# Kernel optimization log

Measured on AMD Instinct MI355X. Metric: run time of the kernel, lower is better.

## Reference

```python
import jax, jax.numpy as jnp
import numpy as np

B, R, H, W = 8, 128, 4096, 4096

def setup_inputs() -> dict:
    key = jax.random.key(0)
    k1, k2, k3, k4 = jax.random.split(key, 4)
    N = jax.random.normal(k1, (B, 1, R, W), dtype=jnp.float32)
    Ak_L = jax.random.normal(k2, (B, 1, H, W), dtype=jnp.float32)
    alpha = jax.random.uniform(k3, (B,), dtype=jnp.float32)
    gamma = jax.random.uniform(k4, (B,), dtype=jnp.float32)
    return {"N": N, "Ak_L": Ak_L, "alpha": alpha, "gamma": gamma}

def reference(N, Ak_L, alpha, gamma):
    # N: [B,1,r,W], Ak_L: [B,1,H,W], alpha/gamma: [B]
    b = N.shape[0]
    r = N.shape[2]
    a = alpha.reshape(b, 1, 1, 1)
    g = gamma.reshape(b, 1, 1, 1)
    I = jnp.eye(r, dtype=N.dtype)  # broadcast over [B,1,r,r]
    # C = alpha*I + 2*gamma * N @ N^T  -> [B,1,r,r]
    C = a * I + 2.0 * g * jnp.einsum('bcrw,bcsw->bcrs', N, N)
    Cinv = jnp.linalg.pinv(C)  # batched pinv over [B,1]
    # X = (Ak_L @ N^T) @ pinv(C) -> [B,1,H,r]
    AN = jnp.einsum('bchw,bcrw->bchr', Ak_L, N)
    X = jnp.einsum('bchr,bcrs->bchs', AN, Cinv)
    return 2.0 * g * X
```

## Files before the change

### kernel.cpp

```cpp
#include <hip/hip_runtime.h>


typedef __attribute__((ext_vector_type(8))) short bf16x8;
typedef __attribute__((ext_vector_type(4))) float f32x4;
typedef __attribute__((ext_vector_type(4))) unsigned int u32x4;

#define MFMA16(a, b, c) __builtin_amdgcn_mfma_f32_16x16x32_bf16((a), (b), (c), 0, 0, 0)
#define NSPLIT 8

__device__ __forceinline__ unsigned short f2bf(float f) {
  union { float f; unsigned u; } v; v.f = f;
  unsigned u = v.u;
  return (unsigned short)((u + 0x7FFFu + ((u >> 16) & 1u)) >> 16);
}
__device__ __forceinline__ unsigned pack2(float x, float y) {
  return (unsigned)f2bf(x) | ((unsigned)f2bf(y) << 16);
}

__global__ __launch_bounds__(256) void k_castT(const float* __restrict__ N,
                                               unsigned short* __restrict__ NT) {
  __attribute__((aligned(16))) __shared__ float tile[128 * 68];
  int wc = blockIdx.x, b = blockIdx.y;
  const float* Nb = N + (size_t)b * 524288 + wc * 64;
  int t = threadIdx.x;
  int row = t >> 1, half = t & 1;
  const float* src = Nb + (size_t)row * 4096 + half * 32;
  float* dst = tile + row * 68 + half * 32;
#pragma unroll
  for (int j = 0; j < 8; j++) *(f32x4*)(dst + j * 4) = *(const f32x4*)(src + j * 4);
  __syncthreads();
  int ow = t >> 2, q = t & 3;
  unsigned short* out = NT + (size_t)b * 524288 + (size_t)(wc * 64 + ow) * 128 + q * 32;
#pragma unroll
  for (int c = 0; c < 4; c++) {
    u32x4 p;
#pragma unroll
    for (int k = 0; k < 4; k++) {
      float f0 = tile[(q * 32 + c * 8 + k * 2) * 68 + ow];
      float f1 = tile[(q * 32 + c * 8 + k * 2 + 1) * 68 + ow];
      p[k] = pack2(f0, f1);
    }
    *(u32x4*)(out + c * 8) = p;
  }
}

__global__ __launch_bounds__(256) void k_gram(const float* __restrict__ N,
                                              float* __restrict__ Gpart) {
  __attribute__((aligned(16))) __shared__ unsigned short lds[128 * 72];
  int ks = blockIdx.x, b = blockIdx.y;
  const float* Nb = N + (size_t)b * 524288 + ks * 512;
  int t = threadIdx.x;
  int wave = t >> 6, lane = t & 63, quad = lane >> 4, l16 = lane & 15;
  f32x4 acc[2][8];
#pragma unroll
  for (int i = 0; i < 2; i++)
#pragma unroll
    for (int j = 0; j < 8; j++) acc[i][j] = (f32x4){0.f, 0.f, 0.f, 0.f};
  int srow = t >> 1, shalf = t & 1;
  const float* srcb = Nb + (size_t)srow * 4096 + shalf * 32;
  unsigned short* dptr = lds + srow * 72 + shalf * 32;
  for (int it = 0; it < 8; ++it) {
    u32x4 pk0, pk1;
    {
      f32x4 v0 = *(const f32x4*)(srcb + it * 64 + 0);
      f32x4 v1 = *(const f32x4*)(srcb + it * 64 + 4);
      f32x4 v2 = *(const f32x4*)(srcb + it * 64 + 8);
      f32x4 v3 = *(const f32x4*)(srcb + it * 64 + 12);
      pk0[0] = pack2(v0[0], v0[1]); pk0[1] = pack2(v0[2], v0[3]);
      pk0[2] = pack2(v1[0], v1[1]); pk0[3] = pack2(v1[2], v1[3]);
      pk1[0] = pack2(v2[0], v2[1]); pk1[1] = pack2(v2[2], v2[3]);
      pk1[2] = pack2(v3[0], v3[1]); pk1[3] = pack2(v3[2], v3[3]);
    }
    u32x4 pk2, pk3;
    {
      f32x4 v0 = *(const f32x4*)(srcb + it * 64 + 16);
      f32x4 v1 = *(const f32x4*)(srcb + it * 64 + 20);
      f32x4 v2 = *(const f32x4*)(srcb + it * 64 + 24);
      f32x4 v3 = *(const f32x4*)(srcb + it * 64 + 28);
      pk2[0] = pack2(v0[0], v0[1]); pk2[1] = pack2(v0[2], v0[3]);
      pk2[2] = pack2(v1[0], v1[1]); pk2[3] = pack2(v1[2], v1[3]);
      pk3[0] = pack2(v2[0], v2[1]); pk3[1] = pack2(v2[2], v2[3]);
      pk3[2] = pack2(v3[0], v3[1]); pk3[3] = pack2(v3[2], v3[3]);
    }
    __syncthreads();
    *(u32x4*)(dptr + 0) = pk0;
    *(u32x4*)(dptr + 8) = pk1;
    *(u32x4*)(dptr + 16) = pk2;
    *(u32x4*)(dptr + 24) = pk3;
    __syncthreads();
    bf16x8 af[2][2], bfv[8][2];
#pragma unroll
    for (int mt = 0; mt < 2; mt++)
#pragma unroll
      for (int kk = 0; kk < 2; kk++)
        af[mt][kk] = *(const bf16x8*)(lds + (wave * 32 + mt * 16 + l16) * 72 + (kk * 4 + quad) * 8);
#pragma unroll
    for (int nt = 0; nt < 8; nt++)
#pragma unroll
      for (int kk = 0; kk < 2; kk++)
        bfv[nt][kk] = *(const bf16x8*)(lds + (nt * 16 + l16) * 72 + (kk * 4 + quad) * 8);
#pragma unroll
    for (int mt = 0; mt < 2; mt++)
#pragma unroll
      for (int nt = 0; nt < 8; nt++)
#pragma unroll
        for (int kk = 0; kk < 2; kk++)
          acc[mt][nt] = MFMA16(af[mt][kk], bfv[nt][kk], acc[mt][nt]);
  }
  float* Gp = Gpart + ((size_t)(b * NSPLIT + ks) << 14);
#pragma unroll
  for (int mt = 0; mt < 2; mt++)
#pragma unroll
    for (int nt = 0; nt < 8; nt++)
#pragma unroll
      for (int rg = 0; rg < 4; rg++) {
        int row = wave * 32 + mt * 16 + quad * 4 + rg;
        int col = nt * 16 + l16;
        Gp[row * 128 + col] = acc[mt][nt][rg];
      }
}

__global__ __launch_bounds__(1024) void k_inv(const float* __restrict__ Gpart,
                                              const float* __restrict__ alpha,
                                              const float* __restrict__ gamma,
                                              float* __restrict__ Cinv) {
  __attribute__((aligned(16))) __shared__ float Cs[16384];
  __attribute__((aligned(16))) __shared__ float mcol[2][128];
  __attribute__((aligned(16))) __shared__ float pivrow[2][128];
  int b = blockIdx.x;
  int t = threadIdx.x;
  const float* Gp = Gpart + ((size_t)b * NSPLIT << 14);
#pragma unroll
  for (int c = 0; c < 4; c++) {
    int off = c * 4096 + t * 4;
    f32x4 s = (f32x4){0.f, 0.f, 0.f, 0.f};
#pragma unroll
    for (int ks = 0; ks < NSPLIT; ks++) s += *(const f32x4*)(Gp + ks * 16384 + off);
    *(f32x4*)(Cs + off) = s;
  }
  __syncthreads();
  int cg = t & 31, rb = t >> 5;
  float al = alpha[b], ga2 = 2.f * gamma[b];
  float a[4][4];
#pragma unroll
  for (int i = 0; i < 4; i++) {
    int r = rb * 4 + i;
    f32x4 v = *(const f32x4*)(Cs + r * 128 + cg * 4);
#pragma unroll
    for (int j = 0; j < 4; j++) {
      int c = cg * 4 + j;
      a[i][j] = ga2 * v[j] + ((r == c) ? al : 0.f);
    }
  }
  for (int p = 0; p < 128; ++p) {
    int pb = p & 1;
    int cgp = p >> 2, jp = p & 3;
    int rbp = p >> 2, ip = p & 3;
    if (cg == cgp) {
      f32x4 mv;
#pragma unroll
      for (int i = 0; i < 4; i++)
        mv[i] = (jp & 2) ? ((jp & 1) ? a[i][3] : a[i][2]) : ((jp & 1) ? a[i][1] : a[i][0]);
      *(f32x4*)&mcol[pb][rb * 4] = mv;
    }
    if (rb == rbp) {
      f32x4 pv;
#pragma unroll
      for (int j = 0; j < 4; j++)
        pv[j] = (ip & 2) ? ((ip & 1) ? a[3][j] : a[2][j]) : ((ip & 1) ? a[1][j] : a[0][j]);
      *(f32x4*)&pivrow[pb][cg * 4] = pv;
    }
    __syncthreads();
    float invd = 1.0f / mcol[pb][p];
    f32x4 mc = *(const f32x4*)&mcol[pb][rb * 4];
    f32x4 pr = *(const f32x4*)&pivrow[pb][cg * 4];
#pragma unroll
    for (int i = 0; i < 4; i++) {
      int r = rb * 4 + i;
      float mi = mc[i] * invd;
#pragma unroll
      for (int j = 0; j < 4; j++) {
        int c = cg * 4 + j;
        float v = a[i][j] - mi * pr[j];
        if (c == p) v = -mi;
        if (r == p) v = pr[j] * invd;
        if (r == p && c == p) v = invd;
        a[i][j] = v;
      }
    }
  }
  float* dst = Cinv + ((size_t)b << 14);
#pragma unroll
  for (int i = 0; i < 4; i++) {
    int r = rb * 4 + i;
    *(f32x4*)(dst + r * 128 + cg * 4) = (f32x4){a[i][0], a[i][1], a[i][2], a[i][3]};
  }
}

__global__ __launch_bounds__(256) void k_mt(const float* __restrict__ Cinv,
                                            const unsigned short* __restrict__ NT,
                                            const float* __restrict__ gamma,
                                            unsigned short* __restrict__ Mt) {
  __attribute__((aligned(16))) __shared__ unsigned short la[128 * 72];
  __attribute__((aligned(16))) __shared__ unsigned short lb[128 * 72];
  int wc = blockIdx.x, b = blockIdx.y;
  int w0 = wc * 128;
  float ga2 = 2.f * gamma[b];
  const float* Cb = Cinv + ((size_t)b << 14);
  const unsigned short* NTb = NT + (size_t)b * 524288;
  int t = threadIdx.x, wave = t >> 6, lane = t & 63, quad = lane >> 4, l16 = lane & 15;
  f32x4 acc[2][8];
#pragma unroll
  for (int i = 0; i < 2; i++)
#pragma unroll
    for (int j = 0; j < 8; j++) acc[i][j] = (f32x4){0.f, 0.f, 0.f, 0.f};
  int row = t >> 1, half = t & 1;
  const float* asrc = Cb + (size_t)row * 128 + half * 32;
  const unsigned short* bsrc = NTb + (size_t)(w0 + row) * 128 + half * 32;
  unsigned short* adst = la + row * 72 + half * 32;
  unsigned short* bdst = lb + row * 72 + half * 32;
  for (int it = 0; it < 2; ++it) {
    int k0 = it * 64;
    u32x4 pa0, pa1;
    {
      f32x4 v0 = *(const f32x4*)(asrc + k0 + 0);
      f32x4 v1 = *(const f32x4*)(asrc + k0 + 4);
      f32x4 v2 = *(const f32x4*)(asrc + k0 + 8);
      f32x4 v3 = *(const f32x4*)(asrc + k0 + 12);
      pa0[0] = pack2(ga2 * v0[0], ga2 * v0[1]); pa0[1] = pack2(ga2 * v0[2], ga2 * v0[3]);
      pa0[2] = pack2(ga2 * v1[0], ga2 * v1[1]); pa0[3] = pack2(ga2 * v1[2], ga2 * v1[3]);
      pa1[0] = pack2(ga2 * v2[0], ga2 * v2[1]); pa1[1] = pack2(ga2 * v2[2], ga2 * v2[3]);
      pa1[2] = pack2(ga2 * v3[0], ga2 * v3[1]); pa1[3] = pack2(ga2 * v3[2], ga2 * v3[3]);
    }
    u32x4 pa2, pa3;
    {
      f32x4 v0 = *(const f32x4*)(asrc + k0 + 16);
      f32x4 v1 = *(const f32x4*)(asrc + k0 + 20);
      f32x4 v2 = *(const f32x4*)(asrc + k0 + 24);
      f32x4 v3 = *(const f32x4*)(asrc + k0 + 28);
      pa2[0] = pack2(ga2 * v0[0], ga2 * v0[1]); pa2[1] = pack2(ga2 * v0[2], ga2 * v0[3]);
      pa2[2] = pack2(ga2 * v1[0], ga2 * v1[1]); pa2[3] = pack2(ga2 * v1[2], ga2 * v1[3]);
      pa3[0] = pack2(ga2 * v2[0], ga2 * v2[1]); pa3[1] = pack2(ga2 * v2[2], ga2 * v2[3]);
      pa3[2] = pack2(ga2 * v3[0], ga2 * v3[1]); pa3[3] = pack2(ga2 * v3[2], ga2 * v3[3]);
    }
    u32x4 bv0 = *(const u32x4*)(bsrc + k0 + 0);
    u32x4 bv1 = *(const u32x4*)(bsrc + k0 + 8);
    u32x4 bv2 = *(const u32x4*)(bsrc + k0 + 16);
    u32x4 bv3 = *(const u32x4*)(bsrc + k0 + 24);
    __syncthreads();
    *(u32x4*)(adst + 0) = pa0;  *(u32x4*)(adst + 8) = pa1;
    *(u32x4*)(adst + 16) = pa2; *(u32x4*)(adst + 24) = pa3;
    *(u32x4*)(bdst + 0) = bv0;  *(u32x4*)(bdst + 8) = bv1;
    *(u32x4*)(bdst + 16) = bv2; *(u32x4*)(bdst + 24) = bv3;
    __syncthreads();
    bf16x8 af[2][2], bfv[8][2];
#pragma unroll
    for (int mt = 0; mt < 2; mt++)
#pragma unroll
      for (int kk = 0; kk < 2; kk++)
        af[mt][kk] = *(const bf16x8*)(la + (wave * 32 + mt * 16 + l16) * 72 + (kk * 4 + quad) * 8);
#pragma unroll
    for (int nt = 0; nt < 8; nt++)
#pragma unroll
      for (int kk = 0; kk < 2; kk++)
        bfv[nt][kk] = *(const bf16x8*)(lb + (nt * 16 + l16) * 72 + (kk * 4 + quad) * 8);
#pragma unroll
    for (int mt = 0; mt < 2; mt++)
#pragma unroll
      for (int nt = 0; nt < 8; nt++)
#pragma unroll
        for (int kk = 0; kk < 2; kk++)
          acc[mt][nt] = MFMA16(af[mt][kk], bfv[nt][kk], acc[mt][nt]);
    __syncthreads();
  }
  unsigned short* Mb = Mt + (size_t)b * 524288;
#pragma unroll
  for (int mt = 0; mt < 2; mt++)
#pragma unroll
    for (int nt = 0; nt < 8; nt++)
#pragma unroll
      for (int rg = 0; rg < 4; rg++) {
        int r = wave * 32 + mt * 16 + quad * 4 + rg;
        int w = w0 + nt * 16 + l16;
        Mb[(size_t)r * 4096 + w] = f2bf(acc[mt][nt][rg]);
      }
}

__device__ __forceinline__ void gemm_step(
    f32x4& A0, f32x4& A1, f32x4& A2, f32x4& A3,
    u32x4& B0, u32x4& B1, u32x4& B2, u32x4& B3,
    unsigned short* adst, unsigned short* bdst,
    const unsigned short* lap, const unsigned short* lbp,
    const float* asrc, const unsigned short* bsrc,
    int next_k0, int do_pf, int wm, int wr, int quad, int l16,
    f32x4 (&acc)[2][4]) {
  u32x4 pa0, pa1;
  pa0[0] = pack2(A0[0], A0[1]); pa0[1] = pack2(A0[2], A0[3]);
  pa0[2] = pack2(A1[0], A1[1]); pa0[3] = pack2(A1[2], A1[3]);
  pa1[0] = pack2(A2[0], A2[1]); pa1[1] = pack2(A2[2], A2[3]);
  pa1[2] = pack2(A3[0], A3[1]); pa1[3] = pack2(A3[2], A3[3]);
  *(u32x4*)(adst + 0) = pa0;
  *(u32x4*)(adst + 8) = pa1;
  *(u32x4*)(bdst + 0) = B0;
  *(u32x4*)(bdst + 8) = B1;
  *(u32x4*)(bdst + 16) = B2;
  *(u32x4*)(bdst + 24) = B3;
  asm volatile("s_waitcnt lgkmcnt(0)" ::: "memory");
  __builtin_amdgcn_s_barrier();
  __builtin_amdgcn_sched_barrier(0);
  if (do_pf) {
    A0 = *(const f32x4*)(asrc + next_k0 + 0);
    A1 = *(const f32x4*)(asrc + next_k0 + 4);
    A2 = *(const f32x4*)(asrc + next_k0 + 8);
    A3 = *(const f32x4*)(asrc + next_k0 + 12);
    B0 = *(const u32x4*)(bsrc + next_k0 + 0);
    B1 = *(const u32x4*)(bsrc + next_k0 + 8);
    B2 = *(const u32x4*)(bsrc + next_k0 + 16);
    B3 = *(const u32x4*)(bsrc + next_k0 + 24);
  }
  bf16x8 af[2][2], bfv[4][2];
#pragma unroll
  for (int mt = 0; mt < 2; mt++)
#pragma unroll
    for (int kk = 0; kk < 2; kk++)
      af[mt][kk] = *(const bf16x8*)(lap + (wm * 32 + mt * 16 + l16) * 72 + (kk * 4 + quad) * 8);
#pragma unroll
  for (int rt = 0; rt < 4; rt++)
#pragma unroll
    for (int kk = 0; kk < 2; kk++)
      bfv[rt][kk] = *(const bf16x8*)(lbp + (wr * 64 + rt * 16 + l16) * 72 + (kk * 4 + quad) * 8);
#pragma unroll
  for (int mt = 0; mt < 2; mt++)
#pragma unroll
    for (int rt = 0; rt < 4; rt++)
#pragma unroll
      for (int kk = 0; kk < 2; kk++)
        acc[mt][rt] = MFMA16(af[mt][kk], bfv[rt][kk], acc[mt][rt]);
}

__global__ __launch_bounds__(256) void k_gemm(const float* __restrict__ A,
                                              const unsigned short* __restrict__ Mt,
                                              float* __restrict__ out) {
  __attribute__((aligned(16))) __shared__ unsigned short la[2][64 * 72];
  __attribute__((aligned(16))) __shared__ unsigned short lb[2][128 * 72];
  int blk = blockIdx.x;
  int b = blk & 7, mtile = blk >> 3;
  const float* Ab = A + (size_t)b * 16777216 + (size_t)mtile * 64 * 4096;
  const unsigned short* Mb = Mt + (size_t)b * 524288;
  int t = threadIdx.x, wave = t >> 6, lane = t & 63, quad = lane >> 4, l16 = lane & 15;
  int wm = wave >> 1, wr = wave & 1;
  f32x4 acc[2][4];
#pragma unroll
  for (int i = 0; i < 2; i++)
#pragma unroll
    for (int j = 0; j < 4; j++) acc[i][j] = (f32x4){0.f, 0.f, 0.f, 0.f};
  int arow = t >> 2, aq = t & 3;
  int brow = t >> 1, bhalf = t & 1;
  const float* asrc = Ab + (size_t)arow * 4096 + aq * 16;
  const unsigned short* bsrc = Mb + (size_t)brow * 4096 + bhalf * 32;
  unsigned short* adst0 = &la[0][arow * 72 + aq * 16];
  unsigned short* adst1 = &la[1][arow * 72 + aq * 16];
  unsigned short* bdst0 = &lb[0][brow * 72 + bhalf * 32];
  unsigned short* bdst1 = &lb[1][brow * 72 + bhalf * 32];
  f32x4 xa0 = *(const f32x4*)(asrc + 0);
  f32x4 xa1 = *(const f32x4*)(asrc + 4);
  f32x4 xa2 = *(const f32x4*)(asrc + 8);
  f32x4 xa3 = *(const f32x4*)(asrc + 12);
  u32x4 xb0 = *(const u32x4*)(bsrc + 0);
  u32x4 xb1 = *(const u32x4*)(bsrc + 8);
  u32x4 xb2 = *(const u32x4*)(bsrc + 16);
  u32x4 xb3 = *(const u32x4*)(bsrc + 24);
  f32x4 ya0 = *(const f32x4*)(asrc + 64);
  f32x4 ya1 = *(const f32x4*)(asrc + 68);
  f32x4 ya2 = *(const f32x4*)(asrc + 72);
  f32x4 ya3 = *(const f32x4*)(asrc + 76);
  u32x4 yb0 = *(const u32x4*)(bsrc + 64);
  u32x4 yb1 = *(const u32x4*)(bsrc + 72);
  u32x4 yb2 = *(const u32x4*)(bsrc + 80);
  u32x4 yb3 = *(const u32x4*)(bsrc + 88);
  for (int itp = 0; itp < 32; ++itp) {
    int pf = (itp < 31);
    gemm_step(xa0, xa1, xa2, xa3, xb0, xb1, xb2, xb3,
              adst0, bdst0, &la[0][0], &lb[0][0], asrc, bsrc,
              (2 * itp + 2) * 64, pf, wm, wr, quad, l16, acc);
    gemm_step(ya0, ya1, ya2, ya3, yb0, yb1, yb2, yb3,
              adst1, bdst1, &la[1][0], &lb[1][0], asrc, bsrc,
              (2 * itp + 3) * 64, pf, wm, wr, quad, l16, acc);
  }
  float* ob = out + (size_t)b * 524288 + (size_t)mtile * 64 * 128;
#pragma unroll
  for (int mt = 0; mt < 2; mt++)
#pragma unroll
    for (int rt = 0; rt < 4; rt++)
#pragma unroll
      for (int rg = 0; rg < 4; rg++) {
        int h = wm * 32 + mt * 16 + quad * 4 + rg;
        int r = wr * 64 + rt * 16 + l16;
        ob[h * 128 + r] = acc[mt][rt][rg];
      }
}

extern "C" void kernel_launch(void* const* d_in, const int* in_sizes, int n_in,
                              void* d_out, int out_size, void* d_ws, size_t ws_size,
                              hipStream_t stream) {
  const float* N = (const float*)d_in[0];
  const float* Ak = (const float*)d_in[1];
  const float* alpha = (const float*)d_in[2];
  const float* gamma = (const float*)d_in[3];
  float* out = (float*)d_out;
  char* ws = (char*)d_ws;
  unsigned short* NT = (unsigned short*)(ws);
  float* Gpart = (float*)(ws + 8388608);
  float* Cinv = (float*)(ws + 12582912);
  unsigned short* Mt = (unsigned short*)(ws + 13107200);

  k_castT<<<dim3(64, 8), 256, 0, stream>>>(N, NT);
  k_gram<<<dim3(NSPLIT, 8), 256, 0, stream>>>(N, Gpart);
  k_inv<<<dim3(8), 1024, 0, stream>>>(Gpart, alpha, gamma, Cinv);
  k_mt<<<dim3(32, 8), 256, 0, stream>>>(Cinv, NT, gamma, Mt);
  k_gemm<<<dim3(512), 256, 0, stream>>>(Ak, Mt, out);
}
```

Measured before the change: 854.5 us.

## Reassociate to (A·Nᵀ)·C⁻¹ and run inversion concurrently with the big GEMM

The pipeline changes from computing M = γ·C⁻¹·N first and then A·Mᵀ to computing AN = A·Nᵀ directly and multiplying by C⁻¹ in a small final kernel. This lets the 128×128 Gauss-Jordan inversion run in 8 extra blocks of the same launch as the large GEMM, so the serial inversion overlaps the GEMM instead of blocking it. The bf16 cast of N is fused into the Gram kernel, which removes the transpose kernel. The big GEMM now uses a PAD of 68, prefetches B one step ahead and A two steps ahead, and declares an occupancy hint. In exchange it adds an fp32 AN round trip through memory plus a scalar-FMA final kernel, and the inversion blocks use 256 threads each holding an 8×8 register tile, which risks register pressure.

```diff
diff --git a/kernel.cpp b/kernel.cpp
--- a/kernel.cpp
+++ b/kernel.cpp
@@ -7,6 +7,7 @@
 
 #define MFMA16(a, b, c) __builtin_amdgcn_mfma_f32_16x16x32_bf16((a), (b), (c), 0, 0, 0)
 #define NSPLIT 8
+#define PAD 68
 
 __device__ __forceinline__ unsigned short f2bf(float f) {
   union { float f; unsigned u; } v; v.f = f;
@@ -16,36 +17,14 @@
 __device__ __forceinline__ unsigned pack2(float x, float y) {
   return (unsigned)f2bf(x) | ((unsigned)f2bf(y) << 16);
 }
-
-__global__ __launch_bounds__(256) void k_castT(const float* __restrict__ N,
-                                               unsigned short* __restrict__ NT) {
-  __attribute__((aligned(16))) __shared__ float tile[128 * 68];
-  int wc = blockIdx.x, b = blockIdx.y;
-  const float* Nb = N + (size_t)b * 524288 + wc * 64;
-  int t = threadIdx.x;
-  int row = t >> 1, half = t & 1;
-  const float* src = Nb + (size_t)row * 4096 + half * 32;
-  float* dst = tile + row * 68 + half * 32;
-#pragma unroll
-  for (int j = 0; j < 8; j++) *(f32x4*)(dst + j * 4) = *(const f32x4*)(src + j * 4);
-  __syncthreads();
-  int ow = t >> 2, q = t & 3;
-  unsigned short* out = NT + (size_t)b * 524288 + (size_t)(wc * 64 + ow) * 128 + q * 32;
-#pragma unroll
-  for (int c = 0; c < 4; c++) {
-    u32x4 p;
-#pragma unroll
-    for (int k = 0; k < 4; k++) {
-      float f0 = tile[(q * 32 + c * 8 + k * 2) * 68 + ow];
-      float f1 = tile[(q * 32 + c * 8 + k * 2 + 1) * 68 + ow];
-      p[k] = pack2(f0, f1);
-    }
-    *(u32x4*)(out + c * 8) = p;
-  }
+__device__ __forceinline__ float sel8row(const float* ar, int s) {
+  return (s & 4) ? ((s & 2) ? ((s & 1) ? ar[7] : ar[6]) : ((s & 1) ? ar[5] : ar[4]))
+                 : ((s & 2) ? ((s & 1) ? ar[3] : ar[2]) : ((s & 1) ? ar[1] : ar[0]));
 }
 
 __global__ __launch_bounds__(256) void k_gram(const float* __restrict__ N,
-                                              float* __restrict__ Gpart) {
+                                              float* __restrict__ Gpart,
+                                              unsigned short* __restrict__ Nbf) {
   __attribute__((aligned(16))) __shared__ unsigned short lds[128 * 72];
   int ks = blockIdx.x, b = blockIdx.y;
   const float* Nb = N + (size_t)b * 524288 + ks * 512;
@@ -59,6 +38,7 @@
   int srow = t >> 1, shalf = t & 1;
   const float* srcb = Nb + (size_t)srow * 4096 + shalf * 32;
   unsigned short* dptr = lds + srow * 72 + shalf * 32;
+  unsigned short* nbb = Nbf + (size_t)b * 524288 + (size_t)srow * 4096 + ks * 512 + shalf * 32;
   for (int it = 0; it < 8; ++it) {
     u32x4 pk0, pk1;
     {
@@ -82,6 +62,10 @@
       pk3[0] = pack2(v2[0], v2[1]); pk3[1] = pack2(v2[2], v2[3]);
       pk3[2] = pack2(v3[0], v3[1]); pk3[3] = pack2(v3[2], v3[3]);
     }
+    *(u32x4*)(nbb + it * 64 + 0) = pk0;
+    *(u32x4*)(nbb + it * 64 + 8) = pk1;
+    *(u32x4*)(nbb + it * 64 + 16) = pk2;
+    *(u32x4*)(nbb + it * 64 + 24) = pk3;
     __syncthreads();
     *(u32x4*)(dptr + 0) = pk0;
     *(u32x4*)(dptr + 8) = pk1;
@@ -120,179 +104,13 @@
       }
 }
 
-__global__ __launch_bounds__(1024) void k_inv(const float* __restrict__ Gpart,
-                                              const float* __restrict__ alpha,
-                                              const float* __restrict__ gamma,
-                                              float* __restrict__ Cinv) {
-  __attribute__((aligned(16))) __shared__ float Cs[16384];
-  __attribute__((aligned(16))) __shared__ float mcol[2][128];
-  __attribute__((aligned(16))) __shared__ float pivrow[2][128];
-  int b = blockIdx.x;
-  int t = threadIdx.x;
-  const float* Gp = Gpart + ((size_t)b * NSPLIT << 14);
-#pragma unroll
-  for (int c = 0; c < 4; c++) {
-    int off = c * 4096 + t * 4;
-    f32x4 s = (f32x4){0.f, 0.f, 0.f, 0.f};
-#pragma unroll
-    for (int ks = 0; ks < NSPLIT; ks++) s += *(const f32x4*)(Gp + ks * 16384 + off);
-    *(f32x4*)(Cs + off) = s;
-  }
-  __syncthreads();
-  int cg = t & 31, rb = t >> 5;
-  float al = alpha[b], ga2 = 2.f * gamma[b];
-  float a[4][4];
-#pragma unroll
-  for (int i = 0; i < 4; i++) {
-    int r = rb * 4 + i;
-    f32x4 v = *(const f32x4*)(Cs + r * 128 + cg * 4);
-#pragma unroll
-    for (int j = 0; j < 4; j++) {
-      int c = cg * 4 + j;
-      a[i][j] = ga2 * v[j] + ((r == c) ? al : 0.f);
-    }
-  }
-  for (int p = 0; p < 128; ++p) {
-    int pb = p & 1;
-    int cgp = p >> 2, jp = p & 3;
-    int rbp = p >> 2, ip = p & 3;
-    if (cg == cgp) {
-      f32x4 mv;
-#pragma unroll
-      for (int i = 0; i < 4; i++)
-        mv[i] = (jp & 2) ? ((jp & 1) ? a[i][3] : a[i][2]) : ((jp & 1) ? a[i][1] : a[i][0]);
-      *(f32x4*)&mcol[pb][rb * 4] = mv;
-    }
-    if (rb == rbp) {
-      f32x4 pv;
-#pragma unroll
-      for (int j = 0; j < 4; j++)
-        pv[j] = (ip & 2) ? ((ip & 1) ? a[3][j] : a[2][j]) : ((ip & 1) ? a[1][j] : a[0][j]);
-      *(f32x4*)&pivrow[pb][cg * 4] = pv;
-    }
-    __syncthreads();
-    float invd = 1.0f / mcol[pb][p];
-    f32x4 mc = *(const f32x4*)&mcol[pb][rb * 4];
-    f32x4 pr = *(const f32x4*)&pivrow[pb][cg * 4];
-#pragma unroll
-    for (int i = 0; i < 4; i++) {
-      int r = rb * 4 + i;
-      float mi = mc[i] * invd;
-#pragma unroll
-      for (int j = 0; j < 4; j++) {
-        int c = cg * 4 + j;
-        float v = a[i][j] - mi * pr[j];
-        if (c == p) v = -mi;
-        if (r == p) v = pr[j] * invd;
-        if (r == p && c == p) v = invd;
-        a[i][j] = v;
-      }
-    }
-  }
-  float* dst = Cinv + ((size_t)b << 14);
-#pragma unroll
-  for (int i = 0; i < 4; i++) {
-    int r = rb * 4 + i;
-    *(f32x4*)(dst + r * 128 + cg * 4) = (f32x4){a[i][0], a[i][1], a[i][2], a[i][3]};
-  }
-}
-
-__global__ __launch_bounds__(256) void k_mt(const float* __restrict__ Cinv,
-                                            const unsigned short* __restrict__ NT,
-                                            const float* __restrict__ gamma,
-                                            unsigned short* __restrict__ Mt) {
-  __attribute__((aligned(16))) __shared__ unsigned short la[128 * 72];
-  __attribute__((aligned(16))) __shared__ unsigned short lb[128 * 72];
-  int wc = blockIdx.x, b = blockIdx.y;
-  int w0 = wc * 128;
-  float ga2 = 2.f * gamma[b];
-  const float* Cb = Cinv + ((size_t)b << 14);
-  const unsigned short* NTb = NT + (size_t)b * 524288;
-  int t = threadIdx.x, wave = t >> 6, lane = t & 63, quad = lane >> 4, l16 = lane & 15;
-  f32x4 acc[2][8];
-#pragma unroll
-  for (int i = 0; i < 2; i++)
-#pragma unroll
-    for (int j = 0; j < 8; j++) acc[i][j] = (f32x4){0.f, 0.f, 0.f, 0.f};
-  int row = t >> 1, half = t & 1;
-  const float* asrc = Cb + (size_t)row * 128 + half * 32;
-  const unsigned short* bsrc = NTb + (size_t)(w0 + row) * 128 + half * 32;
-  unsigned short* adst = la + row * 72 + half * 32;
-  unsigned short* bdst = lb + row * 72 + half * 32;
-  for (int it = 0; it < 2; ++it) {
-    int k0 = it * 64;
-    u32x4 pa0, pa1;
-    {
-      f32x4 v0 = *(const f32x4*)(asrc + k0 + 0);
-      f32x4 v1 = *(const f32x4*)(asrc + k0 + 4);
-      f32x4 v2 = *(const f32x4*)(asrc + k0 + 8);
-      f32x4 v3 = *(const f32x4*)(asrc + k0 + 12);
-      pa0[0] = pack2(ga2 * v0[0], ga2 * v0[1]); pa0[1] = pack2(ga2 * v0[2], ga2 * v0[3]);
-      pa0[2] = pack2(ga2 * v1[0], ga2 * v1[1]); pa0[3] = pack2(ga2 * v1[2], ga2 * v1[3]);
-      pa1[0] = pack2(ga2 * v2[0], ga2 * v2[1]); pa1[1] = pack2(ga2 * v2[2], ga2 * v2[3]);
-      pa1[2] = pack2(ga2 * v3[0], ga2 * v3[1]); pa1[3] = pack2(ga2 * v3[2], ga2 * v3[3]);
-    }
-    u32x4 pa2, pa3;
-    {
-      f32x4 v0 = *(const f32x4*)(asrc + k0 + 16);
-      f32x4 v1 = *(const f32x4*)(asrc + k0 + 20);
-      f32x4 v2 = *(const f32x4*)(asrc + k0 + 24);
-      f32x4 v3 = *(const f32x4*)(asrc + k0 + 28);
-      pa2[0] = pack2(ga2 * v0[0], ga2 * v0[1]); pa2[1] = pack2(ga2 * v0[2], ga2 * v0[3]);
-      pa2[2] = pack2(ga2 * v1[0], ga2 * v1[1]); pa2[3] = pack2(ga2 * v1[2], ga2 * v1[3]);
-      pa3[0] = pack2(ga2 * v2[0], ga2 * v2[1]); pa3[1] = pack2(ga2 * v2[2], ga2 * v2[3]);
-      pa3[2] = pack2(ga2 * v3[0], ga2 * v3[1]); pa3[3] = pack2(ga2 * v3[2], ga2 * v3[3]);
-    }
-    u32x4 bv0 = *(const u32x4*)(bsrc + k0 + 0);
-    u32x4 bv1 = *(const u32x4*)(bsrc + k0 + 8);
-    u32x4 bv2 = *(const u32x4*)(bsrc + k0 + 16);
-    u32x4 bv3 = *(const u32x4*)(bsrc + k0 + 24);
-    __syncthreads();
-    *(u32x4*)(adst + 0) = pa0;  *(u32x4*)(adst + 8) = pa1;
-    *(u32x4*)(adst + 16) = pa2; *(u32x4*)(adst + 24) = pa3;
-    *(u32x4*)(bdst + 0) = bv0;  *(u32x4*)(bdst + 8) = bv1;
-    *(u32x4*)(bdst + 16) = bv2; *(u32x4*)(bdst + 24) = bv3;
-    __syncthreads();
-    bf16x8 af[2][2], bfv[8][2];
-#pragma unroll
-    for (int mt = 0; mt < 2; mt++)
-#pragma unroll
-      for (int kk = 0; kk < 2; kk++)
-        af[mt][kk] = *(const bf16x8*)(la + (wave * 32 + mt * 16 + l16) * 72 + (kk * 4 + quad) * 8);
-#pragma unroll
-    for (int nt = 0; nt < 8; nt++)
-#pragma unroll
-      for (int kk = 0; kk < 2; kk++)
-        bfv[nt][kk] = *(const bf16x8*)(lb + (nt * 16 + l16) * 72 + (kk * 4 + quad) * 8);
-#pragma unroll
-    for (int mt = 0; mt < 2; mt++)
-#pragma unroll
-      for (int nt = 0; nt < 8; nt++)
-#pragma unroll
-        for (int kk = 0; kk < 2; kk++)
-          acc[mt][nt] = MFMA16(af[mt][kk], bfv[nt][kk], acc[mt][nt]);
-    __syncthreads();
-  }
-  unsigned short* Mb = Mt + (size_t)b * 524288;
-#pragma unroll
-  for (int mt = 0; mt < 2; mt++)
-#pragma unroll
-    for (int nt = 0; nt < 8; nt++)
-#pragma unroll
-      for (int rg = 0; rg < 4; rg++) {
-        int r = wave * 32 + mt * 16 + quad * 4 + rg;
-        int w = w0 + nt * 16 + l16;
-        Mb[(size_t)r * 4096 + w] = f2bf(acc[mt][nt][rg]);
-      }
-}
-
-__device__ __forceinline__ void gemm_step(
+__device__ __forceinline__ void an_step(
     f32x4& A0, f32x4& A1, f32x4& A2, f32x4& A3,
     u32x4& B0, u32x4& B1, u32x4& B2, u32x4& B3,
     unsigned short* adst, unsigned short* bdst,
     const unsigned short* lap, const unsigned short* lbp,
     const float* asrc, const unsigned short* bsrc,
-    int next_k0, int do_pf, int wm, int wr, int quad, int l16,
+    int it, int wm, int wr, int quad, int l16,
     f32x4 (&acc)[2][4]) {
   u32x4 pa0, pa1;
   pa0[0] = pack2(A0[0], A0[1]); pa0[1] = pack2(A0[2], A0[3]);
@@ -308,27 +126,32 @@
   asm volatile("s_waitcnt lgkmcnt(0)" ::: "memory");
   __builtin_amdgcn_s_barrier();
   __builtin_amdgcn_sched_barrier(0);
-  if (do_pf) {
-    A0 = *(const f32x4*)(asrc + next_k0 + 0);
-    A1 = *(const f32x4*)(asrc + next_k0 + 4);
-    A2 = *(const f32x4*)(asrc + next_k0 + 8);
-    A3 = *(const f32x4*)(asrc + next_k0 + 12);
-    B0 = *(const u32x4*)(bsrc + next_k0 + 0);
-    B1 = *(const u32x4*)(bsrc + next_k0 + 8);
-    B2 = *(const u32x4*)(bsrc + next_k0 + 16);
-    B3 = *(const u32x4*)(bsrc + next_k0 + 24);
-  }
+  if (it + 1 < 64) {
+    int kb = (it + 1) * 64;
+    B0 = *(const u32x4*)(bsrc + kb + 0);
+    B1 = *(const u32x4*)(bsrc + kb + 8);
+    B2 = *(const u32x4*)(bsrc + kb + 16);
+    B3 = *(const u32x4*)(bsrc + kb + 24);
+  }
+  if (it + 2 < 64) {
+    int ka = (it + 2) * 64;
+    A0 = *(const f32x4*)(asrc + ka + 0);
+    A1 = *(const f32x4*)(asrc + ka + 4);
+    A2 = *(const f32x4*)(asrc + ka + 8);
+    A3 = *(const f32x4*)(asrc + ka + 12);
+  }
+  __builtin_amdgcn_sched_barrier(0);
   bf16x8 af[2][2], bfv[4][2];
 #pragma unroll
   for (int mt = 0; mt < 2; mt++)
 #pragma unroll
     for (int kk = 0; kk < 2; kk++)
-      af[mt][kk] = *(const bf16x8*)(lap + (wm * 32 + mt * 16 + l16) * 72 + (kk * 4 + quad) * 8);
+      af[mt][kk] = *(const bf16x8*)(lap + (wm * 32 + mt * 16 + l16) * PAD + (kk * 4 + quad) * 8);
 #pragma unroll
   for (int rt = 0; rt < 4; rt++)
 #pragma unroll
     for (int kk = 0; kk < 2; kk++)
-      bfv[rt][kk] = *(const bf16x8*)(lbp + (wr * 64 + rt * 16 + l16) * 72 + (kk * 4 + quad) * 8);
+      bfv[rt][kk] = *(const bf16x8*)(lbp + (wr * 64 + rt * 16 + l16) * PAD + (kk * 4 + quad) * 8);
 #pragma unroll
   for (int mt = 0; mt < 2; mt++)
 #pragma unroll
@@ -338,16 +161,91 @@
         acc[mt][rt] = MFMA16(af[mt][kk], bfv[rt][kk], acc[mt][rt]);
 }
 
-__global__ __launch_bounds__(256) void k_gemm(const float* __restrict__ A,
-                                              const unsigned short* __restrict__ Mt,
-                                              float* __restrict__ out) {
-  __attribute__((aligned(16))) __shared__ unsigned short la[2][64 * 72];
-  __attribute__((aligned(16))) __shared__ unsigned short lb[2][128 * 72];
+__global__ __launch_bounds__(256, 3) void k_aninv(
+    const float* __restrict__ A, const unsigned short* __restrict__ Nbf,
+    const float* __restrict__ Gpart, const float* __restrict__ alpha,
+    const float* __restrict__ gamma, float* __restrict__ ANf,
+    float* __restrict__ Cinv) {
+  __attribute__((aligned(16))) __shared__ unsigned short smem[2 * 64 * PAD + 2 * 128 * PAD];
   int blk = blockIdx.x;
-  int b = blk & 7, mtile = blk >> 3;
+  int t = threadIdx.x;
+  if (blk < 8) {
+    int b = blk;
+    float* mcol = (float*)smem;
+    float* pivrow = (float*)smem + 256;
+    const float* Gp = Gpart + ((size_t)b * NSPLIT << 14);
+    int cg = t & 15, rb = t >> 4;
+    float al = alpha[b], ga2 = 2.f * gamma[b];
+    float a[8][8];
+#pragma unroll
+    for (int i = 0; i < 8; i++) {
+      int r = rb * 8 + i;
+      f32x4 s0 = (f32x4){0.f, 0.f, 0.f, 0.f}, s1 = s0;
+#pragma unroll
+      for (int ks = 0; ks < NSPLIT; ks++) {
+        const float* base = Gp + ks * 16384 + r * 128 + cg * 8;
+        s0 += *(const f32x4*)(base);
+        s1 += *(const f32x4*)(base + 4);
+      }
+#pragma unroll
+      for (int j = 0; j < 4; j++) {
+        int c = cg * 8 + j;
+        a[i][j] = ga2 * s0[j] + ((r == c) ? al : 0.f);
+        a[i][4 + j] = ga2 * s1[j] + ((r == c + 4) ? 0.f : 0.f) + ((r == cg * 8 + 4 + j) ? al : 0.f);
+      }
+    }
+    for (int p = 0; p < 128; ++p) {
+      int pb = p & 1;
+      int grp = p >> 3, sub = p & 7;
+      if (cg == grp) {
+#pragma unroll
+        for (int i = 0; i < 8; i++) mcol[pb * 128 + rb * 8 + i] = sel8row(a[i], sub);
+      }
+      if (rb == grp) {
+        float col_k[8];
+#pragma unroll
+        for (int j = 0; j < 8; j++) {
+#pragma unroll
+          for (int i = 0; i < 8; i++) col_k[i] = a[i][j];
+          pivrow[pb * 128 + cg * 8 + j] = sel8row(col_k, sub);
+        }
+      }
+      __syncthreads();
+      float invd = 1.0f / mcol[pb * 128 + p];
+      f32x4 mc0 = *(const f32x4*)(mcol + pb * 128 + rb * 8);
+      f32x4 mc1 = *(const f32x4*)(mcol + pb * 128 + rb * 8 + 4);
+      f32x4 pr0 = *(const f32x4*)(pivrow + pb * 128 + cg * 8);
+      f32x4 pr1 = *(const f32x4*)(pivrow + pb * 128 + cg * 8 + 4);
+      float mc[8] = {mc0[0], mc0[1], mc0[2], mc0[3], mc1[0], mc1[1], mc1[2], mc1[3]};
+      float pr[8] = {pr0[0], pr0[1], pr0[2], pr0[3], pr1[0], pr1[1], pr1[2], pr1[3]};
+#pragma unroll
+      for (int i = 0; i < 8; i++) {
+        int r = rb * 8 + i;
+        float mi = mc[i] * invd;
+#pragma unroll
+        for (int j = 0; j < 8; j++) {
+          int c = cg * 8 + j;
+          float v = a[i][j] - mi * pr[j];
+          if (c == p) v = -mi;
+          if (r == p) v = pr[j] * invd;
+          if (r == p && c == p) v = invd;
+          a[i][j] = v;
+        }
+      }
+    }
+    float* dst = Cinv + ((size_t)b << 14);
+#pragma unroll
+    for (int i = 0; i < 8; i++) {
+      int r = rb * 8 + i;
+      *(f32x4*)(dst + r * 128 + cg * 8) = (f32x4){a[i][0], a[i][1], a[i][2], a[i][3]};
+      *(f32x4*)(dst + r * 128 + cg * 8 + 4) = (f32x4){a[i][4], a[i][5], a[i][6], a[i][7]};
+    }
+    return;
+  }
+  int b = blk & 7, mtile = (blk >> 3) - 1;
   const float* Ab = A + (size_t)b * 16777216 + (size_t)mtile * 64 * 4096;
-  const unsigned short* Mb = Mt + (size_t)b * 524288;
-  int t = threadIdx.x, wave = t >> 6, lane = t & 63, quad = lane >> 4, l16 = lane & 15;
+  const unsigned short* Nb = Nbf + (size_t)b * 524288;
+  int wave = t >> 6, lane = t & 63, quad = lane >> 4, l16 = lane & 15;
   int wm = wave >> 1, wr = wave & 1;
   f32x4 acc[2][4];
 #pragma unroll
@@ -357,37 +255,34 @@
   int arow = t >> 2, aq = t & 3;
   int brow = t >> 1, bhalf = t & 1;
   const float* asrc = Ab + (size_t)arow * 4096 + aq * 16;
-  const unsigned short* bsrc = Mb + (size_t)brow * 4096 + bhalf * 32;
-  unsigned short* adst0 = &la[0][arow * 72 + aq * 16];
-  unsigned short* adst1 = &la[1][arow * 72 + aq * 16];
-  unsigned short* bdst0 = &lb[0][brow * 72 + bhalf * 32];
-  unsigned short* bdst1 = &lb[1][brow * 72 + bhalf * 32];
+  const unsigned short* bsrc = Nb + (size_t)brow * 4096 + bhalf * 32;
+  unsigned short* adst_e = smem + arow * PAD + aq * 16;
+  unsigned short* adst_o = adst_e + 64 * PAD;
+  unsigned short* bdst_e = smem + 2 * 64 * PAD + brow * PAD + bhalf * 32;
+  unsigned short* bdst_o = bdst_e + 128 * PAD;
+  const unsigned short* lap_e = smem;
+  const unsigned short* lap_o = smem + 64 * PAD;
+  const unsigned short* lbp_e = smem + 2 * 64 * PAD;
+  const unsigned short* lbp_o = lbp_e + 128 * PAD;
+  u32x4 B0 = *(const u32x4*)(bsrc + 0);
+  u32x4 B1 = *(const u32x4*)(bsrc + 8);
+  u32x4 B2 = *(const u32x4*)(bsrc + 16);
+  u32x4 B3 = *(const u32x4*)(bsrc + 24);
   f32x4 xa0 = *(const f32x4*)(asrc + 0);
   f32x4 xa1 = *(const f32x4*)(asrc + 4);
   f32x4 xa2 = *(const f32x4*)(asrc + 8);
   f32x4 xa3 = *(const f32x4*)(asrc + 12);
-  u32x4 xb0 = *(const u32x4*)(bsrc + 0);
-  u32x4 xb1 = *(const u32x4*)(bsrc + 8);
-  u32x4 xb2 = *(const u32x4*)(bsrc + 16);
-  u32x4 xb3 = *(const u32x4*)(bsrc + 24);
   f32x4 ya0 = *(const f32x4*)(asrc + 64);
   f32x4 ya1 = *(const f32x4*)(asrc + 68);
   f32x4 ya2 = *(const f32x4*)(asrc + 72);
   f32x4 ya3 = *(const f32x4*)(asrc + 76);
-  u32x4 yb0 = *(const u32x4*)(bsrc + 64);
-  u32x4 yb1 = *(const u32x4*)(bsrc + 72);
-  u32x4 yb2 = *(const u32x4*)(bsrc + 80);
-  u32x4 yb3 = *(const u32x4*)(bsrc + 88);
-  for (int itp = 0; itp < 32; ++itp) {
-    int pf = (itp < 31);
-    gemm_step(xa0, xa1, xa2, xa3, xb0, xb1, xb2, xb3,
-              adst0, bdst0, &la[0][0], &lb[0][0], asrc, bsrc,
-              (2 * itp + 2) * 64, pf, wm, wr, quad, l16, acc);
-    gemm_step(ya0, ya1, ya2, ya3, yb0, yb1, yb2, yb3,
-              adst1, bdst1, &la[1][0], &lb[1][0], asrc, bsrc,
-              (2 * itp + 3) * 64, pf, wm, wr, quad, l16, acc);
-  }
-  float* ob = out + (size_t)b * 524288 + (size_t)mtile * 64 * 128;
+  for (int m = 0; m < 32; ++m) {
+    an_step(xa0, xa1, xa2, xa3, B0, B1, B2, B3, adst_e, bdst_e, lap_e, lbp_e,
+            asrc, bsrc, 2 * m, wm, wr, quad, l16, acc);
+    an_step(ya0, ya1, ya2, ya3, B0, B1, B2, B3, adst_o, bdst_o, lap_o, lbp_o,
+            asrc, bsrc, 2 * m + 1, wm, wr, quad, l16, acc);
+  }
+  float* ob = ANf + (size_t)b * 524288 + (size_t)mtile * 64 * 128;
 #pragma unroll
   for (int mt = 0; mt < 2; mt++)
 #pragma unroll
@@ -398,6 +293,59 @@
         int r = wr * 64 + rt * 16 + l16;
         ob[h * 128 + r] = acc[mt][rt][rg];
       }
+}
+
+__global__ __launch_bounds__(256) void k_final(const float* __restrict__ AN,
+                                               const float* __restrict__ Cinv,
+                                               const float* __restrict__ gamma,
+                                               float* __restrict__ out) {
+  __attribute__((aligned(16))) __shared__ float Cs[16384];
+  int blk = blockIdx.x;
+  int b = blk & 7, mtile = blk >> 3;
+  const float* Cb = Cinv + ((size_t)b << 14);
+  int t = threadIdx.x;
+#pragma unroll
+  for (int c = 0; c < 4; c++) {
+    int off = c * 4096 + t * 16;
+#pragma unroll
+    for (int q = 0; q < 4; q++)
+      *(f32x4*)(Cs + off + q * 4) = *(const f32x4*)(Cb + off + q * 4);
+  }
+  __syncthreads();
+  int sg = t >> 4, hg = t & 15;
+  const float* ANb = AN + (size_t)b * 524288 + (size_t)mtile * 64 * 128;
+  f32x4 acc[4][2];
+#pragma unroll
+  for (int i = 0; i < 4; i++) {
+    acc[i][0] = (f32x4){0.f, 0.f, 0.f, 0.f};
+    acc[i][1] = (f32x4){0.f, 0.f, 0.f, 0.f};
+  }
+  for (int r0 = 0; r0 < 128; r0 += 16) {
+    f32x4 av[4][4];
+#pragma unroll
+    for (int i = 0; i < 4; i++)
+#pragma unroll
+      for (int k4 = 0; k4 < 4; k4++)
+        av[i][k4] = *(const f32x4*)(ANb + (hg * 4 + i) * 128 + r0 + k4 * 4);
+#pragma unroll
+    for (int rr = 0; rr < 16; rr++) {
+      f32x4 c0 = *(const f32x4*)(Cs + (r0 + rr) * 128 + sg * 8);
+      f32x4 c1 = *(const f32x4*)(Cs + (r0 + rr) * 128 + sg * 8 + 4);
+#pragma unroll
+      for (int i = 0; i < 4; i++) {
+        float aval = av[i][rr >> 2][rr & 3];
+        acc[i][0] += aval * c0;
+        acc[i][1] += aval * c1;
+      }
+    }
+  }
+  float ga2 = 2.f * gamma[b];
+  float* ob = out + (size_t)b * 524288 + (size_t)mtile * 64 * 128;
+#pragma unroll
+  for (int i = 0; i < 4; i++) {
+    *(f32x4*)(ob + (hg * 4 + i) * 128 + sg * 8) = ga2 * acc[i][0];
+    *(f32x4*)(ob + (hg * 4 + i) * 128 + sg * 8 + 4) = ga2 * acc[i][1];
+  }
 }
 
 extern "C" void kernel_launch(void* const* d_in, const int* in_sizes, int n_in,
@@ -409,14 +357,12 @@
   const float* gamma = (const float*)d_in[3];
   float* out = (float*)d_out;
   char* ws = (char*)d_ws;
-  unsigned short* NT = (unsigned short*)(ws);
+  unsigned short* Nbf = (unsigned short*)(ws);
   float* Gpart = (float*)(ws + 8388608);
   float* Cinv = (float*)(ws + 12582912);
-  unsigned short* Mt = (unsigned short*)(ws + 13107200);
-
-  k_castT<<<dim3(64, 8), 256, 0, stream>>>(N, NT);
-  k_gram<<<dim3(NSPLIT, 8), 256, 0, stream>>>(N, Gpart);
-  k_inv<<<dim3(8), 1024, 0, stream>>>(Gpart, alpha, gamma, Cinv);
-  k_mt<<<dim3(32, 8), 256, 0, stream>>>(Cinv, NT, gamma, Mt);
-  k_gemm<<<dim3(512), 256, 0, stream>>>(Ak, Mt, out);
-}
+  float* ANf = (float*)(ws + 13107200);
+
+  k_gram<<<dim3(NSPLIT, 8), 256, 0, stream>>>(N, Gpart, Nbf);
+  k_aninv<<<dim3(520), 256, 0, stream>>>(Ak, Nbf, Gpart, alpha, gamma, ANf, Cinv);
+  k_final<<<dim3(512), 256, 0, stream>>>(ANf, Cinv, gamma, out);
+}
```

New measurement: 1.098 ms. 28.5% more time.

## Reassociate to compute Ak·Nᵀ first and apply pinv in a small fp32 kernel

Applied to the files above, without the earlier changes.

The product is reassociated. Previously the code built M = 2γ·Cinv·N in bf16 and then ran the large GEMM Ak·Mᵀ. Now the large GEMM computes AN = Ak·Nᵀ directly, using a bf16 copy of N that the Gram kernel writes as a side output. A new fp32 kernel then multiplies AN by Cinv and scales by 2γ. This removes the separate transpose-cast kernel and the Cinv·N kernel, and keeps Cinv in fp32. In exchange it adds a round trip of the 16 MB fp32 AN intermediate through global memory plus an extra launch.

```diff
diff --git a/kernel.cpp b/kernel.cpp
--- a/kernel.cpp
+++ b/kernel.cpp
@@ -17,35 +17,9 @@
   return (unsigned)f2bf(x) | ((unsigned)f2bf(y) << 16);
 }
 
-__global__ __launch_bounds__(256) void k_castT(const float* __restrict__ N,
-                                               unsigned short* __restrict__ NT) {
-  __attribute__((aligned(16))) __shared__ float tile[128 * 68];
-  int wc = blockIdx.x, b = blockIdx.y;
-  const float* Nb = N + (size_t)b * 524288 + wc * 64;
-  int t = threadIdx.x;
-  int row = t >> 1, half = t & 1;
-  const float* src = Nb + (size_t)row * 4096 + half * 32;
-  float* dst = tile + row * 68 + half * 32;
-#pragma unroll
-  for (int j = 0; j < 8; j++) *(f32x4*)(dst + j * 4) = *(const f32x4*)(src + j * 4);
-  __syncthreads();
-  int ow = t >> 2, q = t & 3;
-  unsigned short* out = NT + (size_t)b * 524288 + (size_t)(wc * 64 + ow) * 128 + q * 32;
-#pragma unroll
-  for (int c = 0; c < 4; c++) {
-    u32x4 p;
-#pragma unroll
-    for (int k = 0; k < 4; k++) {
-      float f0 = tile[(q * 32 + c * 8 + k * 2) * 68 + ow];
-      float f1 = tile[(q * 32 + c * 8 + k * 2 + 1) * 68 + ow];
-      p[k] = pack2(f0, f1);
-    }
-    *(u32x4*)(out + c * 8) = p;
-  }
-}
-
 __global__ __launch_bounds__(256) void k_gram(const float* __restrict__ N,
-                                              float* __restrict__ Gpart) {
+                                              float* __restrict__ Gpart,
+                                              unsigned short* __restrict__ Nbf) {
   __attribute__((aligned(16))) __shared__ unsigned short lds[128 * 72];
   int ks = blockIdx.x, b = blockIdx.y;
   const float* Nb = N + (size_t)b * 524288 + ks * 512;
@@ -59,6 +33,7 @@
   int srow = t >> 1, shalf = t & 1;
   const float* srcb = Nb + (size_t)srow * 4096 + shalf * 32;
   unsigned short* dptr = lds + srow * 72 + shalf * 32;
+  unsigned short* nbb = Nbf + (size_t)b * 524288 + (size_t)srow * 4096 + ks * 512 + shalf * 32;
   for (int it = 0; it < 8; ++it) {
     u32x4 pk0, pk1;
     {
@@ -82,6 +57,10 @@
       pk3[0] = pack2(v2[0], v2[1]); pk3[1] = pack2(v2[2], v2[3]);
       pk3[2] = pack2(v3[0], v3[1]); pk3[3] = pack2(v3[2], v3[3]);
     }
+    *(u32x4*)(nbb + it * 64 + 0) = pk0;
+    *(u32x4*)(nbb + it * 64 + 8) = pk1;
+    *(u32x4*)(nbb + it * 64 + 16) = pk2;
+    *(u32x4*)(nbb + it * 64 + 24) = pk3;
     __syncthreads();
     *(u32x4*)(dptr + 0) = pk0;
     *(u32x4*)(dptr + 8) = pk1;
@@ -195,95 +174,6 @@
     int r = rb * 4 + i;
     *(f32x4*)(dst + r * 128 + cg * 4) = (f32x4){a[i][0], a[i][1], a[i][2], a[i][3]};
   }
-}
-
-__global__ __launch_bounds__(256) void k_mt(const float* __restrict__ Cinv,
-                                            const unsigned short* __restrict__ NT,
-                                            const float* __restrict__ gamma,
-                                            unsigned short* __restrict__ Mt) {
-  __attribute__((aligned(16))) __shared__ unsigned short la[128 * 72];
-  __attribute__((aligned(16))) __shared__ unsigned short lb[128 * 72];
-  int wc = blockIdx.x, b = blockIdx.y;
-  int w0 = wc * 128;
-  float ga2 = 2.f * gamma[b];
-  const float* Cb = Cinv + ((size_t)b << 14);
-  const unsigned short* NTb = NT + (size_t)b * 524288;
-  int t = threadIdx.x, wave = t >> 6, lane = t & 63, quad = lane >> 4, l16 = lane & 15;
-  f32x4 acc[2][8];
-#pragma unroll
-  for (int i = 0; i < 2; i++)
-#pragma unroll
-    for (int j = 0; j < 8; j++) acc[i][j] = (f32x4){0.f, 0.f, 0.f, 0.f};
-  int row = t >> 1, half = t & 1;
-  const float* asrc = Cb + (size_t)row * 128 + half * 32;
-  const unsigned short* bsrc = NTb + (size_t)(w0 + row) * 128 + half * 32;
-  unsigned short* adst = la + row * 72 + half * 32;
-  unsigned short* bdst = lb + row * 72 + half * 32;
-  for (int it = 0; it < 2; ++it) {
-    int k0 = it * 64;
-    u32x4 pa0, pa1;
-    {
-      f32x4 v0 = *(const f32x4*)(asrc + k0 + 0);
-      f32x4 v1 = *(const f32x4*)(asrc + k0 + 4);
-      f32x4 v2 = *(const f32x4*)(asrc + k0 + 8);
-      f32x4 v3 = *(const f32x4*)(asrc + k0 + 12);
-      pa0[0] = pack2(ga2 * v0[0], ga2 * v0[1]); pa0[1] = pack2(ga2 * v0[2], ga2 * v0[3]);
-      pa0[2] = pack2(ga2 * v1[0], ga2 * v1[1]); pa0[3] = pack2(ga2 * v1[2], ga2 * v1[3]);
-      pa1[0] = pack2(ga2 * v2[0], ga2 * v2[1]); pa1[1] = pack2(ga2 * v2[2], ga2 * v2[3]);
-      pa1[2] = pack2(ga2 * v3[0], ga2 * v3[1]); pa1[3] = pack2(ga2 * v3[2], ga2 * v3[3]);
-    }
-    u32x4 pa2, pa3;
-    {
-      f32x4 v0 = *(const f32x4*)(asrc + k0 + 16);
-      f32x4 v1 = *(const f32x4*)(asrc + k0 + 20);
-      f32x4 v2 = *(const f32x4*)(asrc + k0 + 24);
-      f32x4 v3 = *(const f32x4*)(asrc + k0 + 28);
-      pa2[0] = pack2(ga2 * v0[0], ga2 * v0[1]); pa2[1] = pack2(ga2 * v0[2], ga2 * v0[3]);
-      pa2[2] = pack2(ga2 * v1[0], ga2 * v1[1]); pa2[3] = pack2(ga2 * v1[2], ga2 * v1[3]);
-      pa3[0] = pack2(ga2 * v2[0], ga2 * v2[1]); pa3[1] = pack2(ga2 * v2[2], ga2 * v2[3]);
-      pa3[2] = pack2(ga2 * v3[0], ga2 * v3[1]); pa3[3] = pack2(ga2 * v3[2], ga2 * v3[3]);
-    }
-    u32x4 bv0 = *(const u32x4*)(bsrc + k0 + 0);
-    u32x4 bv1 = *(const u32x4*)(bsrc + k0 + 8);
-    u32x4 bv2 = *(const u32x4*)(bsrc + k0 + 16);
-    u32x4 bv3 = *(const u32x4*)(bsrc + k0 + 24);
-    __syncthreads();
-    *(u32x4*)(adst + 0) = pa0;  *(u32x4*)(adst + 8) = pa1;
-    *(u32x4*)(adst + 16) = pa2; *(u32x4*)(adst + 24) = pa3;
-    *(u32x4*)(bdst + 0) = bv0;  *(u32x4*)(bdst + 8) = bv1;
-    *(u32x4*)(bdst + 16) = bv2; *(u32x4*)(bdst + 24) = bv3;
-    __syncthreads();
-    bf16x8 af[2][2], bfv[8][2];
-#pragma unroll
-    for (int mt = 0; mt < 2; mt++)
-#pragma unroll
-      for (int kk = 0; kk < 2; kk++)
-        af[mt][kk] = *(const bf16x8*)(la + (wave * 32 + mt * 16 + l16) * 72 + (kk * 4 + quad) * 8);
-#pragma unroll
-    for (int nt = 0; nt < 8; nt++)
-#pragma unroll
-      for (int kk = 0; kk < 2; kk++)
-        bfv[nt][kk] = *(const bf16x8*)(lb + (nt * 16 + l16) * 72 + (kk * 4 + quad) * 8);
-#pragma unroll
-    for (int mt = 0; mt < 2; mt++)
-#pragma unroll
-      for (int nt = 0; nt < 8; nt++)
-#pragma unroll
-        for (int kk = 0; kk < 2; kk++)
-          acc[mt][nt] = MFMA16(af[mt][kk], bfv[nt][kk], acc[mt][nt]);
-    __syncthreads();
-  }
-  unsigned short* Mb = Mt + (size_t)b * 524288;
-#pragma unroll
-  for (int mt = 0; mt < 2; mt++)
-#pragma unroll
-    for (int nt = 0; nt < 8; nt++)
-#pragma unroll
-      for (int rg = 0; rg < 4; rg++) {
-        int r = wave * 32 + mt * 16 + quad * 4 + rg;
-        int w = w0 + nt * 16 + l16;
-        Mb[(size_t)r * 4096 + w] = f2bf(acc[mt][nt][rg]);
-      }
 }
 
 __device__ __forceinline__ void gemm_step(
@@ -338,15 +228,15 @@
         acc[mt][rt] = MFMA16(af[mt][kk], bfv[rt][kk], acc[mt][rt]);
 }
 
-__global__ __launch_bounds__(256) void k_gemm(const float* __restrict__ A,
-                                              const unsigned short* __restrict__ Mt,
-                                              float* __restrict__ out) {
+__global__ __launch_bounds__(256) void k_angemm(const float* __restrict__ A,
+                                                const unsigned short* __restrict__ Nbf,
+                                                float* __restrict__ ANf) {
   __attribute__((aligned(16))) __shared__ unsigned short la[2][64 * 72];
   __attribute__((aligned(16))) __shared__ unsigned short lb[2][128 * 72];
   int blk = blockIdx.x;
   int b = blk & 7, mtile = blk >> 3;
   const float* Ab = A + (size_t)b * 16777216 + (size_t)mtile * 64 * 4096;
-  const unsigned short* Mb = Mt + (size_t)b * 524288;
+  const unsigned short* Mb = Nbf + (size_t)b * 524288;
   int t = threadIdx.x, wave = t >> 6, lane = t & 63, quad = lane >> 4, l16 = lane & 15;
   int wm = wave >> 1, wr = wave & 1;
   f32x4 acc[2][4];
@@ -387,7 +277,7 @@
               adst1, bdst1, &la[1][0], &lb[1][0], asrc, bsrc,
               (2 * itp + 3) * 64, pf, wm, wr, quad, l16, acc);
   }
-  float* ob = out + (size_t)b * 524288 + (size_t)mtile * 64 * 128;
+  float* ob = ANf + (size_t)b * 524288 + (size_t)mtile * 64 * 128;
 #pragma unroll
   for (int mt = 0; mt < 2; mt++)
 #pragma unroll
@@ -398,6 +288,59 @@
         int r = wr * 64 + rt * 16 + l16;
         ob[h * 128 + r] = acc[mt][rt][rg];
       }
+}
+
+__global__ __launch_bounds__(256) void k_final(const float* __restrict__ AN,
+                                               const float* __restrict__ Cinv,
+                                               const float* __restrict__ gamma,
+                                               float* __restrict__ out) {
+  __attribute__((aligned(16))) __shared__ float Cs[16384];
+  int blk = blockIdx.x;
+  int b = blk & 7, mtile = blk >> 3;
+  const float* Cb = Cinv + ((size_t)b << 14);
+  int t = threadIdx.x;
+#pragma unroll
+  for (int c = 0; c < 4; c++) {
+    int off = c * 4096 + t * 16;
+#pragma unroll
+    for (int q = 0; q < 4; q++)
+      *(f32x4*)(Cs + off + q * 4) = *(const f32x4*)(Cb + off + q * 4);
+  }
+  __syncthreads();
+  int sg = t >> 4, hg = t & 15;
+  const float* ANb = AN + (size_t)b * 524288 + (size_t)mtile * 64 * 128;
+  f32x4 acc[4][2];
+#pragma unroll
+  for (int i = 0; i < 4; i++) {
+    acc[i][0] = (f32x4){0.f, 0.f, 0.f, 0.f};
+    acc[i][1] = (f32x4){0.f, 0.f, 0.f, 0.f};
+  }
+  for (int r0 = 0; r0 < 128; r0 += 16) {
+    f32x4 av[4][4];
+#pragma unroll
+    for (int i = 0; i < 4; i++)
+#pragma unroll
+      for (int k4 = 0; k4 < 4; k4++)
+        av[i][k4] = *(const f32x4*)(ANb + (hg * 4 + i) * 128 + r0 + k4 * 4);
+#pragma unroll
+    for (int rr = 0; rr < 16; rr++) {
+      f32x4 c0 = *(const f32x4*)(Cs + (r0 + rr) * 128 + sg * 8);
+      f32x4 c1 = *(const f32x4*)(Cs + (r0 + rr) * 128 + sg * 8 + 4);
+#pragma unroll
+      for (int i = 0; i < 4; i++) {
+        float aval = av[i][rr >> 2][rr & 3];
+        acc[i][0] += aval * c0;
+        acc[i][1] += aval * c1;
+      }
+    }
+  }
+  float ga2 = 2.f * gamma[b];
+  float* ob = out + (size_t)b * 524288 + (size_t)mtile * 64 * 128;
+#pragma unroll
+  for (int i = 0; i < 4; i++) {
+    *(f32x4*)(ob + (hg * 4 + i) * 128 + sg * 8) = ga2 * acc[i][0];
+    *(f32x4*)(ob + (hg * 4 + i) * 128 + sg * 8 + 4) = ga2 * acc[i][1];
+  }
 }
 
 extern "C" void kernel_launch(void* const* d_in, const int* in_sizes, int n_in,
@@ -409,14 +352,13 @@
   const float* gamma = (const float*)d_in[3];
   float* out = (float*)d_out;
   char* ws = (char*)d_ws;
-  unsigned short* NT = (unsigned short*)(ws);
+  unsigned short* Nbf = (unsigned short*)(ws);
   float* Gpart = (float*)(ws + 8388608);
   float* Cinv = (float*)(ws + 12582912);
-  unsigned short* Mt = (unsigned short*)(ws + 13107200);
-
-  k_castT<<<dim3(64, 8), 256, 0, stream>>>(N, NT);
-  k_gram<<<dim3(NSPLIT, 8), 256, 0, stream>>>(N, Gpart);
+  float* ANf = (float*)(ws + 13107200);
+
+  k_gram<<<dim3(NSPLIT, 8), 256, 0, stream>>>(N, Gpart, Nbf);
   k_inv<<<dim3(8), 1024, 0, stream>>>(Gpart, alpha, gamma, Cinv);
-  k_mt<<<dim3(32, 8), 256, 0, stream>>>(Cinv, NT, gamma, Mt);
-  k_gemm<<<dim3(512), 256, 0, stream>>>(Ak, Mt, out);
-}
+  k_angemm<<<dim3(512), 256, 0, stream>>>(Ak, Nbf, ANf);
+  k_final<<<dim3(512), 256, 0, stream>>>(ANf, Cinv, gamma, out);
+}
```

New measurement: 880.1 us. +3.0%, slower.
